# Performance work log

Hardware: AMD Instinct MI355X
Metric: run time of the kernel (lower is better)

The kernel has to match this reference:

```python
import jax, jax.numpy as jnp
import numpy as np

TAU = 20.0   # membrane time constant (init kwarg tau)
TH = 1.0     # spike threshold (init kwarg threshold)
K = 10.0     # surrogate sigmoid sharpness

B, L = 131072, 400


def setup_inputs() -> dict:
    key = jax.random.key(0)
    I = jax.random.normal(key, (B, L), dtype=jnp.float32)
    return {"I": I}


def reference(I) -> jnp.ndarray:
    """LIF Euler integration over time with surrogate (straight-through) spikes.

    Faithful to the torch loop:
        v <- v + (-v/tau + I_t)
        s_soft = sigmoid(k*(v - th)); s_hard = (v >= th)
        s = stopgrad(s_hard - s_soft) + s_soft
        v <- v * (1 - stopgrad(s))
    Returns the spike raster [B, L]. (The original also returns a ragged
    Python list of per-sample spike latencies, which has data-dependent
    shape and is omitted from the jit-able reference.)
    """
    I_t = jnp.swapaxes(I, 0, 1)  # [L, B] for scan over time

    def step(v, It):
        v = v - v / TAU + It
        s_soft = jax.nn.sigmoid(K * (v - TH))
        s_hard = (v >= TH).astype(v.dtype)
        s = jax.lax.stop_gradient(s_hard - s_soft) + s_soft
        v = v * (1.0 - jax.lax.stop_gradient(s))
        return v, s

    v0 = jnp.zeros(I.shape[0], dtype=I.dtype)
    _, spikes_lb = jax.lax.scan(step, v0, I_t)  # [L, B]
    return jnp.swapaxes(spikes_lb, 0, 1)        # [B, L]
```

## Files before the change

### kernel.cpp

```cpp
#include <hip/hip_runtime.h>


#define LIF_L 400
#define LIF_NV (LIF_L / 4)

__global__ __launch_bounds__(256) void lif_kernel(const float* __restrict__ I,
                                                  float* __restrict__ out,
                                                  int nrows) {
    const int row = blockIdx.x * 256 + threadIdx.x;
    if (row >= nrows) return;

    const float4* __restrict__ in4 = reinterpret_cast<const float4*>(I) + (size_t)row * LIF_NV;
    float4* __restrict__ out4      = reinterpret_cast<float4*>(out)     + (size_t)row * LIF_NV;

    float v = 0.0f;

#pragma unroll 4
    for (int j = 0; j < LIF_NV; ++j) {
        const float4 x = in4[j];
        float4 s;

        v = (v - v / 20.0f) + x.x;
        {
            const bool sp = (v >= 1.0f);
            s.x = sp ? 1.0f : 0.0f;
            v   = sp ? 0.0f : v;
        }
        v = (v - v / 20.0f) + x.y;
        {
            const bool sp = (v >= 1.0f);
            s.y = sp ? 1.0f : 0.0f;
            v   = sp ? 0.0f : v;
        }
        v = (v - v / 20.0f) + x.z;
        {
            const bool sp = (v >= 1.0f);
            s.z = sp ? 1.0f : 0.0f;
            v   = sp ? 0.0f : v;
        }
        v = (v - v / 20.0f) + x.w;
        {
            const bool sp = (v >= 1.0f);
            s.w = sp ? 1.0f : 0.0f;
            v   = sp ? 0.0f : v;
        }

        out4[j] = s;
    }
}

extern "C" void kernel_launch(void* const* d_in, const int* in_sizes, int n_in,
                              void* d_out, int out_size, void* d_ws, size_t ws_size,
                              hipStream_t stream) {
    const float* I = (const float*)d_in[0];
    float* out = (float*)d_out;
    const int nrows = in_sizes[0] / LIF_L;

    const int block = 256;
    const int grid = (nrows + block - 1) / block;
    lif_kernel<<<grid, block, 0, stream>>>(I, out, nrows);
}
```

Baseline: 468.3 us.

## Triple-buffer row loads in registers and replace division with reciprocal FMA sequence

Each thread now keeps three register buffers of four float4 chunks and prefetches chunks ahead of the serial recurrence, so global load latency overlaps with compute. The per-step divide by 20 is replaced with a multiply by 0.05 plus an FMA-based correction meant to reproduce the exact division result. This raises register use per thread and may lower occupancy. The loop is effectively memory bound with strided per-thread rows, so the benefit depends on whether more loads in flight help.

```diff
diff --git a/kernel.cpp b/kernel.cpp
--- a/kernel.cpp
+++ b/kernel.cpp
@@ -2,7 +2,9 @@
 
 
 #define LIF_L 400
-#define LIF_NV (LIF_L / 4)
+#define LIF_NV 100
+#define CHUNK 4
+#define NCHUNK 25
 
 __global__ __launch_bounds__(256) void lif_kernel(const float* __restrict__ I,
                                                   float* __restrict__ out,
@@ -13,40 +15,51 @@
     const float4* __restrict__ in4 = reinterpret_cast<const float4*>(I) + (size_t)row * LIF_NV;
     float4* __restrict__ out4      = reinterpret_cast<float4*>(out)     + (size_t)row * LIF_NV;
 
+    constexpr float RCP = 0.05f;
     float v = 0.0f;
 
-#pragma unroll 4
-    for (int j = 0; j < LIF_NV; ++j) {
-        const float4 x = in4[j];
-        float4 s;
+    float4 bA[CHUNK], bB[CHUNK], bC[CHUNK];
 
-        v = (v - v / 20.0f) + x.x;
-        {
-            const bool sp = (v >= 1.0f);
-            s.x = sp ? 1.0f : 0.0f;
-            v   = sp ? 0.0f : v;
+    auto loadChunk = [&](float4* buf, int c) {
+#pragma unroll
+        for (int j = 0; j < CHUNK; ++j) buf[j] = in4[c * CHUNK + j];
+    };
+
+    auto step = [&](float x) -> float {
+        const float p0 = v * RCP;
+        const float e  = __builtin_fmaf(-20.0f, p0, v);
+        const float t  = __builtin_fmaf(e, RCP, p0);
+        v = (v - t) + x;
+        const bool sp = (v >= 1.0f);
+        const float s = sp ? 1.0f : 0.0f;
+        v = sp ? 0.0f : v;
+        return s;
+    };
+
+    auto doChunk = [&](float4* buf, int c) {
+#pragma unroll
+        for (int j = 0; j < CHUNK; ++j) {
+            const float4 x = buf[j];
+            float4 s;
+            s.x = step(x.x);
+            s.y = step(x.y);
+            s.z = step(x.z);
+            s.w = step(x.w);
+            out4[c * CHUNK + j] = s;
         }
-        v = (v - v / 20.0f) + x.y;
-        {
-            const bool sp = (v >= 1.0f);
-            s.y = sp ? 1.0f : 0.0f;
-            v   = sp ? 0.0f : v;
-        }
-        v = (v - v / 20.0f) + x.z;
-        {
-            const bool sp = (v >= 1.0f);
-            s.z = sp ? 1.0f : 0.0f;
-            v   = sp ? 0.0f : v;
-        }
-        v = (v - v / 20.0f) + x.w;
-        {
-            const bool sp = (v >= 1.0f);
-            s.w = sp ? 1.0f : 0.0f;
-            v   = sp ? 0.0f : v;
-        }
+    };
 
-        out4[j] = s;
+    loadChunk(bA, 0);
+    loadChunk(bB, 1);
+    loadChunk(bC, 2);
+
+    for (int k = 0; k < 8; ++k) {
+        const int c = 3 * k;
+        doChunk(bA, c);     loadChunk(bA, c + 3);
+        doChunk(bB, c + 1); if (k < 7) loadChunk(bB, c + 4);
+        doChunk(bC, c + 2); if (k < 7) loadChunk(bC, c + 5);
     }
+    doChunk(bA, 24);
 }
 
 extern "C" void kernel_launch(void* const* d_in, const int* in_sizes, int n_in,
```

After: 439.9 us. 1.06x faster.

## Software-pipeline row loads/stores with inline asm and manual vmcnt waits

Applied to the files above, without the earlier changes.

Replaces the compiler-scheduled per-float4 loop with a hand-pipelined scheme. Each row is split into 25 chunks of 64 bytes, five chunks of loads are kept in flight through inline global_load_dwordx4, and s_waitcnt counts are computed by hand. Stores are also issued through inline asm with a six-deep store buffer. The division by 20 is replaced by a reciprocal multiply plus an FMA correction step, intended to stay bit-exact. This raises VGPR use and depends on the wait counts being correct, and any mistake there would be a silent ordering bug.

```diff
diff --git a/kernel.cpp b/kernel.cpp
--- a/kernel.cpp
+++ b/kernel.cpp
@@ -1,8 +1,9 @@
 #include <hip/hip_runtime.h>
 
 
+typedef float f32x4 __attribute__((ext_vector_type(4)));
+
 #define LIF_L 400
-#define LIF_NV (LIF_L / 4)
 
 __global__ __launch_bounds__(256) void lif_kernel(const float* __restrict__ I,
                                                   float* __restrict__ out,
@@ -10,43 +11,84 @@
     const int row = blockIdx.x * 256 + threadIdx.x;
     if (row >= nrows) return;
 
-    const float4* __restrict__ in4 = reinterpret_cast<const float4*>(I) + (size_t)row * LIF_NV;
-    float4* __restrict__ out4      = reinterpret_cast<float4*>(out)     + (size_t)row * LIF_NV;
+    const float* __restrict__ ib = I + (size_t)row * LIF_L;
+    float*       __restrict__ ob = out + (size_t)row * LIF_L;
 
+    constexpr int NC = 25;
+    constexpr int D  = 5;
+    constexpr int SD = 6;
+
+    f32x4 ld[D][4];
+    f32x4 sv[SD][4] = {};
+
+    #pragma unroll
+    for (int c = 0; c < D; ++c) {
+        #pragma unroll
+        for (int j = 0; j < 4; ++j)
+            asm volatile("global_load_dwordx4 %0, %1, off offset:%c2"
+                         : "=v"(ld[c][j])
+                         : "v"(ib), "i"(c * 64 + j * 16));
+    }
+
+    constexpr int W[NC] = {16, 20, 24, 28, 32,
+                           32, 32, 32, 32, 32, 32, 32, 32,
+                           32, 32, 32, 32, 32, 32, 32, 32,
+                           28, 24, 20, 16};
+
+    constexpr float RCP = 0.05f;
     float v = 0.0f;
 
-#pragma unroll 4
-    for (int j = 0; j < LIF_NV; ++j) {
-        const float4 x = in4[j];
-        float4 s;
+    #pragma unroll
+    for (int c = 0; c < NC; ++c) {
+        const int ls = c % D;
+        const int ss = c % SD;
 
-        v = (v - v / 20.0f) + x.x;
-        {
-            const bool sp = (v >= 1.0f);
-            s.x = sp ? 1.0f : 0.0f;
-            v   = sp ? 0.0f : v;
-        }
-        v = (v - v / 20.0f) + x.y;
-        {
-            const bool sp = (v >= 1.0f);
-            s.y = sp ? 1.0f : 0.0f;
-            v   = sp ? 0.0f : v;
-        }
-        v = (v - v / 20.0f) + x.z;
-        {
-            const bool sp = (v >= 1.0f);
-            s.z = sp ? 1.0f : 0.0f;
-            v   = sp ? 0.0f : v;
-        }
-        v = (v - v / 20.0f) + x.w;
-        {
-            const bool sp = (v >= 1.0f);
-            s.w = sp ? 1.0f : 0.0f;
-            v   = sp ? 0.0f : v;
+        asm volatile("s_waitcnt vmcnt(%c8)"
+                     : "+v"(ld[ls][0]), "+v"(ld[ls][1]),
+                       "+v"(ld[ls][2]), "+v"(ld[ls][3]),
+                       "+v"(sv[ss][0]), "+v"(sv[ss][1]),
+                       "+v"(sv[ss][2]), "+v"(sv[ss][3])
+                     : "i"(W[c]));
+
+        #pragma unroll
+        for (int j = 0; j < 4; ++j) {
+            const f32x4 x = ld[ls][j];
+            f32x4 s;
+            #pragma unroll
+            for (int e = 0; e < 4; ++e) {
+                const float p0 = v * RCP;
+                const float er = __builtin_fmaf(-20.0f, p0, v);
+                const float t  = __builtin_fmaf(er, RCP, p0);
+                v = (v - t) + x[e];
+                const bool sp = (v >= 1.0f);
+                s[e] = sp ? 1.0f : 0.0f;
+                v = sp ? 0.0f : v;
+            }
+            sv[ss][j] = s;
         }
 
-        out4[j] = s;
+        #pragma unroll
+        for (int j = 0; j < 4; ++j)
+            asm volatile("global_store_dwordx4 %0, %1, off offset:%c2"
+                         :: "v"(ob), "v"(sv[ss][j]), "i"(c * 64 + j * 16)
+                         : "memory");
+
+        if (c + D < NC) {
+            #pragma unroll
+            for (int j = 0; j < 4; ++j)
+                asm volatile("global_load_dwordx4 %0, %1, off offset:%c2"
+                             : "=v"(ld[ls][j])
+                             : "v"(ib), "i"((c + D) * 64 + j * 16));
+        }
     }
+
+    asm volatile("s_waitcnt vmcnt(0)"
+                 : "+v"(sv[0][0]), "+v"(sv[0][1]), "+v"(sv[0][2]), "+v"(sv[0][3]),
+                   "+v"(sv[1][0]), "+v"(sv[1][1]), "+v"(sv[1][2]), "+v"(sv[1][3]),
+                   "+v"(sv[2][0]), "+v"(sv[2][1]), "+v"(sv[2][2]), "+v"(sv[2][3]),
+                   "+v"(sv[3][0]), "+v"(sv[3][1]), "+v"(sv[3][2]), "+v"(sv[3][3]),
+                   "+v"(sv[4][0]), "+v"(sv[4][1]), "+v"(sv[4][2]), "+v"(sv[4][3]),
+                   "+v"(sv[5][0]), "+v"(sv[5][1]), "+v"(sv[5][2]), "+v"(sv[5][3]));
 }
 
 extern "C" void kernel_launch(void* const* d_in, const int* in_sizes, int n_in,
```

Measured after the change: 436.0 us. 1.07x faster.
